# Kernel optimization log

Hardware: AMD Instinct MI355X
Metric: run time of the kernel (lower is better)

The kernel has to match this reference:

```python
import jax, jax.numpy as jnp
import numpy as np

NEG_INF = -jnp.inf


def setup_inputs() -> dict:
    B, T, D = 2, 512, 256
    key = jax.random.key(0)
    ks = jax.random.split(key, 12)
    inp = {
        'x': jax.random.normal(ks[0], (B, T, D), jnp.float32),
        'last_x': jnp.zeros((B, 1, D), jnp.float32),
        'last_num': jnp.zeros((B, 1, D), jnp.float32),
        'last_den': jnp.zeros((B, 1, D), jnp.float32),
        'time_decay': jax.random.normal(ks[1], (D,), jnp.float32) * 0.5,
        'time_first': jax.random.normal(ks[2], (D,), jnp.float32) * 0.5,
        'time_mix_k': jax.random.uniform(ks[3], (1, 1, D), jnp.float32),
        'time_mix_v': jax.random.uniform(ks[4], (1, 1, D), jnp.float32),
        'time_mix_r': jax.random.uniform(ks[5], (1, 1, D), jnp.float32),
        'Wk': jax.random.normal(ks[6], (D, D), jnp.float32) * 0.02,
        'Wv': jax.random.normal(ks[7], (D, D), jnp.float32) * 0.02,
        'Wr': jax.random.normal(ks[8], (D, D), jnp.float32) * 0.02,
        'Wo': jax.random.normal(ks[9], (D, D), jnp.float32) * 0.02,
    }
    return inp


def reference(x, last_x, last_num, last_den, time_decay, time_first,
              time_mix_k, time_mix_v, time_mix_r, Wk, Wv, Wr, Wo):
    B, T, D = x.shape

    # time_shift: prepend last_x, drop last step
    xs = jnp.concatenate([last_x, x[:, :-1, :]], axis=1)  # (B,T,D)

    k = (x * time_mix_k + xs * (1.0 - time_mix_k)) @ Wk.T
    v = (x * time_mix_v + xs * (1.0 - time_mix_v)) @ Wv.T
    r = (x * time_mix_r + xs * (1.0 - time_mix_r)) @ Wr.T
    sr = jax.nn.sigmoid(r)

    # --- run_wkv (quadratic exp-masked formulation, faithful to source) ---
    w = -jnp.exp(time_decay)                      # (D,)
    t = jnp.arange(T + 1, dtype=x.dtype)
    # wt[i, j] = j - i
    wt = t[None, :T] - t[:T, None]                # (T,T)
    tw = w[None, :] * t[1:, None]                 # (T,D): w * (j+1)
    twt = w[None, None, :] * wt[:, :, None]       # (T,T,D)
    # causal mask: -inf where j < i (strictly lower triangle, tril_(-1))
    ii = jnp.arange(T)
    mask = jnp.where(ii[:, None] > ii[None, :], NEG_INF, 0.0).astype(x.dtype)
    ktw = twt[None] + k[:, :, None, :] + mask[None, :, :, None]  # (B,T,T,D)
    etw = jnp.exp(tw)                             # (T,D)
    ektw = jnp.exp(ktw)                           # (B,T,T,D)
    num = etw[None] * last_num + jnp.einsum('bijd,bid->bjd', ektw, v)  # (B,T,D)
    den = etw[None] * last_den + ektw.sum(axis=1)                      # (B,T,D)
    num_prev = jnp.concatenate([last_num, num[:, :-1, :]], axis=1)
    den_prev = jnp.concatenate([last_den, den[:, :-1, :]], axis=1)
    euk = jnp.exp(time_first[None, None, :] + k)
    wkv = (num_prev + euk * v) / (den_prev + euk)
    # ----------------------------------------------------------------------

    out = (wkv * sr) @ Wo.T
    return (out, x[:, -1:, :], num[:, -1:, :], den[:, -1:, :])
```

## Files before the change

### kernel.cpp

```cpp
#include <hip/hip_runtime.h>

#define TT 512
#define DD 256
#define BB 2
#define MM (BB*TT)
#define LCH 8

__global__ __launch_bounds__(256)
void gemm_mix_t(const float* __restrict__ X, const float* __restrict__ Xlast,
                const float* __restrict__ W0, const float* __restrict__ W1,
                const float* __restrict__ W2,
                const float* __restrict__ mx0, const float* __restrict__ mx1,
                const float* __restrict__ mx2,
                float* __restrict__ O0, float* __restrict__ O1,
                float* __restrict__ O2)
{
    const int mat = blockIdx.z;
    const float* W  = (mat == 0) ? W0  : (mat == 1) ? W1  : W2;
    const float* mx = (mat == 0) ? mx0 : (mat == 1) ? mx1 : mx2;
    float*       O  = (mat == 0) ? O0  : (mat == 1) ? O1  : O2;

    const int n0   = blockIdx.x * 32;
    const int m0   = blockIdx.y * 32;
    const int b    = m0 / TT;
    const int t0   = m0 % TT;
    const int tid  = threadIdx.x;
    const int wv   = tid >> 6;
    const int lane = tid & 63;

    const int cc = (lane & 7) * 4;
    const int g  = lane >> 3;
    const int tm = lane >> 3;
    const int tn = lane & 7;

    __shared__ float As[4][32][36];
    __shared__ float Bs[4][32][36];

    const int kb = wv * 64;

    float4 a[4], w4[4];
    auto load_chunk = [&](int k0) {
        const float4 mv = *(const float4*)&mx[k0 + cc];
        #pragma unroll
        for (int i = 0; i < 4; ++i) {
            const int rr  = g + 8 * i;
            const int row = m0 + rr;
            const float4 xc = *(const float4*)&X[(size_t)row * DD + k0 + cc];
            float4 xp;
            if (t0 + rr == 0) xp = *(const float4*)&Xlast[b * DD + k0 + cc];
            else              xp = *(const float4*)&X[(size_t)(row - 1) * DD + k0 + cc];
            a[i].x = xp.x + (xc.x - xp.x) * mv.x;
            a[i].y = xp.y + (xc.y - xp.y) * mv.y;
            a[i].z = xp.z + (xc.z - xp.z) * mv.z;
            a[i].w = xp.w + (xc.w - xp.w) * mv.w;
            w4[i] = *(const float4*)&W[(size_t)(n0 + rr) * DD + k0 + cc];
        }
    };

    float acc[4][4] = {};
    load_chunk(kb);

    #pragma unroll
    for (int c = 0; c < 2; ++c) {
        #pragma unroll
        for (int i = 0; i < 4; ++i) {
            const int rr = g + 8 * i;
            As[wv][cc + 0][rr] = a[i].x; As[wv][cc + 1][rr] = a[i].y;
            As[wv][cc + 2][rr] = a[i].z; As[wv][cc + 3][rr] = a[i].w;
            Bs[wv][cc + 0][rr] = w4[i].x; Bs[wv][cc + 1][rr] = w4[i].y;
            Bs[wv][cc + 2][rr] = w4[i].z; Bs[wv][cc + 3][rr] = w4[i].w;
        }
        if (c == 0) load_chunk(kb + 32);
        #pragma unroll
        for (int kk = 0; kk < 32; ++kk) {
            const float4 a4 = *(const float4*)&As[wv][kk][tm * 4];
            const float4 b4 = *(const float4*)&Bs[wv][kk][tn * 4];
            const float am[4] = {a4.x, a4.y, a4.z, a4.w};
            const float bn[4] = {b4.x, b4.y, b4.z, b4.w};
            #pragma unroll
            for (int i = 0; i < 4; ++i)
                #pragma unroll
                for (int j = 0; j < 4; ++j)
                    acc[i][j] = fmaf(am[i], bn[j], acc[i][j]);
        }
    }

    if (wv != 0) {
        float* park = &As[wv][0][0];
        #pragma unroll
        for (int i = 0; i < 4; ++i)
            *(float4*)&park[(i * 64 + lane) * 4] =
                make_float4(acc[i][0], acc[i][1], acc[i][2], acc[i][3]);
    }
    __syncthreads();
    if (wv == 0) {
        #pragma unroll
        for (int w = 1; w < 4; ++w) {
            const float* park = &As[w][0][0];
            #pragma unroll
            for (int i = 0; i < 4; ++i) {
                const float4 o = *(const float4*)&park[(i * 64 + lane) * 4];
                acc[i][0] += o.x; acc[i][1] += o.y;
                acc[i][2] += o.z; acc[i][3] += o.w;
            }
        }
        #pragma unroll
        for (int j = 0; j < 4; ++j) {
            const float4 o = make_float4(acc[0][j], acc[1][j], acc[2][j], acc[3][j]);
            *(float4*)&O[(size_t)(b * DD + n0 + tn * 4 + j) * TT + t0 + tm * 4] = o;
        }
    }
}

__global__ __launch_bounds__(128)
void wkv_scan(const float* __restrict__ kT, const float* __restrict__ vT,
              const float* __restrict__ rT, const float* __restrict__ x,
              const float* __restrict__ last_num, const float* __restrict__ last_den,
              const float* __restrict__ time_decay, const float* __restrict__ time_first,
              float* __restrict__ yT, float* __restrict__ out)
{
    const int tid  = threadIdx.x;
    const int ch   = blockIdx.x * 2 + (tid >> 6);
    const int lane = tid & 63;
    const int b    = ch >> 8;
    const int d    = ch & (DD - 1);

    const float w  = -__expf(time_decay[d]);
    const float ew = __expf(w);
    const float eu = __expf(time_first[d]);

    const size_t base = (size_t)ch * TT + lane * LCH;
    float k_[LCH], v_[LCH], r_[LCH];
    #pragma unroll
    for (int i = 0; i < LCH / 4; ++i) {
        *(float4*)&k_[4 * i] = *(const float4*)(kT + base + 4 * i);
        *(float4*)&v_[4 * i] = *(const float4*)(vT + base + 4 * i);
        *(float4*)&r_[4 * i] = *(const float4*)(rT + base + 4 * i);
    }

    float ek[LCH], ekv[LCH], sr[LCH];
    #pragma unroll
    for (int i = 0; i < LCH; ++i) {
        ek[i]  = __expf(k_[i]);
        ekv[i] = ek[i] * v_[i];
        sr[i]  = __builtin_amdgcn_rcpf(1.0f + __expf(-r_[i]));
    }

    float A = __expf(w * (float)LCH);
    float Bn = 0.0f, Bd = 0.0f;
    #pragma unroll
    for (int i = 0; i < LCH; ++i) {
        Bn = fmaf(ew, Bn, ekv[i]);
        Bd = fmaf(ew, Bd, ek[i]);
    }

    #pragma unroll
    for (int s = 1; s < 64; s <<= 1) {
        const float Ax  = __shfl_up(A, s, 64);
        const float Bnx = __shfl_up(Bn, s, 64);
        const float Bdx = __shfl_up(Bd, s, 64);
        if (lane >= s) {
            Bn = fmaf(A, Bnx, Bn);
            Bd = fmaf(A, Bdx, Bd);
            A *= Ax;
        }
    }

    float Aex  = __shfl_up(A, 1, 64);
    float Bnex = __shfl_up(Bn, 1, 64);
    float Bdex = __shfl_up(Bd, 1, 64);
    if (lane == 0) { Aex = 1.0f; Bnex = 0.0f; Bdex = 0.0f; }
    float sn = fmaf(Aex, last_num[ch], Bnex);
    float sd = fmaf(Aex, last_den[ch], Bdex);

    float y_[LCH];
    #pragma unroll
    for (int i = 0; i < LCH; ++i) {
        const float euk = eu * ek[i];
        const float wkv = (sn + eu * ekv[i]) * __builtin_amdgcn_rcpf(sd + euk);
        y_[i] = wkv * sr[i];
        sn = fmaf(ew, sn, ekv[i]);
        sd = fmaf(ew, sd, ek[i]);
    }
    #pragma unroll
    for (int i = 0; i < LCH / 4; ++i)
        *(float4*)(yT + base + 4 * i) = *(const float4*)&y_[4 * i];

    if (lane == 63) {
        out[MM * DD + BB * DD + ch]     = sn;
        out[MM * DD + 2 * BB * DD + ch] = sd;
    }
    if (lane == 0)
        out[MM * DD + ch] = x[(b * TT + TT - 1) * DD + d];
}

__global__ __launch_bounds__(256)
void gemm_out(const float* __restrict__ yT, const float* __restrict__ Wo,
              float* __restrict__ O)
{
    const int n0   = blockIdx.x * 32;
    const int m0   = blockIdx.y * 32;
    const int b    = m0 >> 9;
    const int t0   = m0 & (TT - 1);
    const int tid  = threadIdx.x;
    const int wv   = tid >> 6;
    const int lane = tid & 63;

    __shared__ float As[4][2][32][40];
    __shared__ float Bs[4][2][32][36];

    const int tm = lane >> 3;
    const int tn = lane & 7;
    const int kr = lane >> 3;
    const int mq = (lane & 7) * 4;
    const int cc = (lane & 7) * 4;
    const int g  = lane >> 3;

    const int kb = wv * 64;

    float4 av[4], wv4[4];
    auto load_chunk = [&](int k0) {
        #pragma unroll
        for (int i = 0; i < 4; ++i)
            av[i] = *(const float4*)&yT[(size_t)(b * DD + k0 + kr + 8 * i) * TT + t0 + mq];
        #pragma unroll
        for (int i = 0; i < 4; ++i)
            wv4[i] = *(const float4*)&Wo[(size_t)(n0 + g + 8 * i) * DD + k0 + cc];
    };

    float acc[4][4] = {};
    load_chunk(kb);

    #pragma unroll
    for (int c = 0; c < 2; ++c) {
        const int buf = c & 1;
        #pragma unroll
        for (int i = 0; i < 4; ++i)
            *(float4*)&As[wv][buf][kr + 8 * i][mq] = av[i];
        #pragma unroll
        for (int i = 0; i < 4; ++i) {
            const int rr = g + 8 * i;
            Bs[wv][buf][cc + 0][rr] = wv4[i].x; Bs[wv][buf][cc + 1][rr] = wv4[i].y;
            Bs[wv][buf][cc + 2][rr] = wv4[i].z; Bs[wv][buf][cc + 3][rr] = wv4[i].w;
        }
        if (c == 0) load_chunk(kb + 32);
        #pragma unroll
        for (int kk = 0; kk < 32; ++kk) {
            const float4 a4 = *(const float4*)&As[wv][buf][kk][tm * 4];
            const float4 b4 = *(const float4*)&Bs[wv][buf][kk][tn * 4];
            const float am[4] = {a4.x, a4.y, a4.z, a4.w};
            const float bn[4] = {b4.x, b4.y, b4.z, b4.w};
            #pragma unroll
            for (int i = 0; i < 4; ++i)
                #pragma unroll
                for (int j = 0; j < 4; ++j)
                    acc[i][j] = fmaf(am[i], bn[j], acc[i][j]);
        }
    }

    if (wv != 0) {
        float* park = &As[wv][0][0][0];
        #pragma unroll
        for (int i = 0; i < 4; ++i)
            *(float4*)&park[lane * 20 + i * 4] =
                make_float4(acc[i][0], acc[i][1], acc[i][2], acc[i][3]);
    }
    __syncthreads();
    if (wv == 0) {
        #pragma unroll
        for (int w = 1; w < 4; ++w) {
            const float* park = &As[w][0][0][0];
            #pragma unroll
            for (int i = 0; i < 4; ++i) {
                const float4 o = *(const float4*)&park[lane * 20 + i * 4];
                acc[i][0] += o.x; acc[i][1] += o.y;
                acc[i][2] += o.z; acc[i][3] += o.w;
            }
        }
        #pragma unroll
        for (int i = 0; i < 4; ++i)
            *(float4*)&O[(size_t)(m0 + tm * 4 + i) * DD + n0 + tn * 4] =
                make_float4(acc[i][0], acc[i][1], acc[i][2], acc[i][3]);
    }
}

extern "C" void kernel_launch(void* const* d_in, const int* in_sizes, int n_in,
                              void* d_out, int out_size, void* d_ws, size_t ws_size,
                              hipStream_t stream)
{
    const float* x    = (const float*)d_in[0];
    const float* lx   = (const float*)d_in[1];
    const float* lnum = (const float*)d_in[2];
    const float* lden = (const float*)d_in[3];
    const float* td   = (const float*)d_in[4];
    const float* tf   = (const float*)d_in[5];
    const float* mk   = (const float*)d_in[6];
    const float* mv   = (const float*)d_in[7];
    const float* mr   = (const float*)d_in[8];
    const float* Wk   = (const float*)d_in[9];
    const float* Wv   = (const float*)d_in[10];
    const float* Wr   = (const float*)d_in[11];
    const float* Wo   = (const float*)d_in[12];
    float* out = (float*)d_out;

    float* kT = (float*)d_ws;
    float* vT = kT + MM * DD;
    float* rT = vT + MM * DD;
    float* yT = rT + MM * DD;

    gemm_mix_t<<<dim3(8, 32, 3), 256, 0, stream>>>(
        x, lx, Wk, Wv, Wr, mk, mv, mr, kT, vT, rT);

    wkv_scan<<<dim3(256), 128, 0, stream>>>(
        kT, vT, rT, x, lnum, lden, td, tf, yT, out);

    gemm_out<<<dim3(8, 32), 256, 0, stream>>>(yT, Wo, out);
}
```

Before: 99.11 us.

## Use packed FP32 FMA in GEMMs and split WKV scan across two wavefronts

Both GEMM inner loops now use inline-asm v_pk_fma_f32, which does two FMAs per instruction through op_sel broadcasting, with accumulators held as float2 pairs. This is meant to halve the VALU issue count in the FMA-bound inner loops. The WKV scan now gives each channel two wavefronts of 4 timesteps per lane instead of one wavefront of 8, and combines the two halves through a small shared-memory carry and a block barrier. This raises parallelism and shortens per-thread serial work, at the cost of an extra sync and more launched threads.

```diff
diff --git a/kernel.cpp b/kernel.cpp
--- a/kernel.cpp
+++ b/kernel.cpp
@@ -4,7 +4,13 @@
 #define DD 256
 #define BB 2
 #define MM (BB*TT)
-#define LCH 8
+
+#define PK_LO(acc, a, b) \
+    asm("v_pk_fma_f32 %0, %1, %2, %0 op_sel:[0,0,0] op_sel_hi:[0,1,1]" \
+        : "+v"(acc) : "v"(a), "v"(b))
+#define PK_HI(acc, a, b) \
+    asm("v_pk_fma_f32 %0, %1, %2, %0 op_sel:[1,0,0] op_sel_hi:[1,1,1]" \
+        : "+v"(acc) : "v"(a), "v"(b))
 
 __global__ __launch_bounds__(256)
 void gemm_mix_t(const float* __restrict__ X, const float* __restrict__ Xlast,
@@ -57,7 +63,7 @@
         }
     };
 
-    float acc[4][4] = {};
+    float2 acc2[4][2] = {};
     load_chunk(kb);
 
     #pragma unroll
@@ -73,15 +79,14 @@
         if (c == 0) load_chunk(kb + 32);
         #pragma unroll
         for (int kk = 0; kk < 32; ++kk) {
-            const float4 a4 = *(const float4*)&As[wv][kk][tm * 4];
-            const float4 b4 = *(const float4*)&Bs[wv][kk][tn * 4];
-            const float am[4] = {a4.x, a4.y, a4.z, a4.w};
-            const float bn[4] = {b4.x, b4.y, b4.z, b4.w};
-            #pragma unroll
-            for (int i = 0; i < 4; ++i)
-                #pragma unroll
-                for (int j = 0; j < 4; ++j)
-                    acc[i][j] = fmaf(am[i], bn[j], acc[i][j]);
+            const float2 a01 = *(const float2*)&As[wv][kk][tm * 4];
+            const float2 a23 = *(const float2*)&As[wv][kk][tm * 4 + 2];
+            const float2 b01 = *(const float2*)&Bs[wv][kk][tn * 4];
+            const float2 b23 = *(const float2*)&Bs[wv][kk][tn * 4 + 2];
+            PK_LO(acc2[0][0], a01, b01); PK_LO(acc2[0][1], a01, b23);
+            PK_HI(acc2[1][0], a01, b01); PK_HI(acc2[1][1], a01, b23);
+            PK_LO(acc2[2][0], a23, b01); PK_LO(acc2[2][1], a23, b23);
+            PK_HI(acc2[3][0], a23, b01); PK_HI(acc2[3][1], a23, b23);
         }
     }
 
@@ -90,7 +95,7 @@
         #pragma unroll
         for (int i = 0; i < 4; ++i)
             *(float4*)&park[(i * 64 + lane) * 4] =
-                make_float4(acc[i][0], acc[i][1], acc[i][2], acc[i][3]);
+                make_float4(acc2[i][0].x, acc2[i][0].y, acc2[i][1].x, acc2[i][1].y);
     }
     __syncthreads();
     if (wv == 0) {
@@ -100,19 +105,22 @@
             #pragma unroll
             for (int i = 0; i < 4; ++i) {
                 const float4 o = *(const float4*)&park[(i * 64 + lane) * 4];
-                acc[i][0] += o.x; acc[i][1] += o.y;
-                acc[i][2] += o.z; acc[i][3] += o.w;
+                acc2[i][0].x += o.x; acc2[i][0].y += o.y;
+                acc2[i][1].x += o.z; acc2[i][1].y += o.w;
             }
         }
-        #pragma unroll
-        for (int j = 0; j < 4; ++j) {
-            const float4 o = make_float4(acc[0][j], acc[1][j], acc[2][j], acc[3][j]);
-            *(float4*)&O[(size_t)(b * DD + n0 + tn * 4 + j) * TT + t0 + tm * 4] = o;
-        }
+        const float4 oj0 = make_float4(acc2[0][0].x, acc2[1][0].x, acc2[2][0].x, acc2[3][0].x);
+        const float4 oj1 = make_float4(acc2[0][0].y, acc2[1][0].y, acc2[2][0].y, acc2[3][0].y);
+        const float4 oj2 = make_float4(acc2[0][1].x, acc2[1][1].x, acc2[2][1].x, acc2[3][1].x);
+        const float4 oj3 = make_float4(acc2[0][1].y, acc2[1][1].y, acc2[2][1].y, acc2[3][1].y);
+        *(float4*)&O[(size_t)(b * DD + n0 + tn * 4 + 0) * TT + t0 + tm * 4] = oj0;
+        *(float4*)&O[(size_t)(b * DD + n0 + tn * 4 + 1) * TT + t0 + tm * 4] = oj1;
+        *(float4*)&O[(size_t)(b * DD + n0 + tn * 4 + 2) * TT + t0 + tm * 4] = oj2;
+        *(float4*)&O[(size_t)(b * DD + n0 + tn * 4 + 3) * TT + t0 + tm * 4] = oj3;
     }
 }
 
-__global__ __launch_bounds__(128)
+__global__ __launch_bounds__(256)
 void wkv_scan(const float* __restrict__ kT, const float* __restrict__ vT,
               const float* __restrict__ rT, const float* __restrict__ x,
               const float* __restrict__ last_num, const float* __restrict__ last_den,
@@ -120,8 +128,10 @@
               float* __restrict__ yT, float* __restrict__ out)
 {
     const int tid  = threadIdx.x;
-    const int ch   = blockIdx.x * 2 + (tid >> 6);
+    const int chl  = tid >> 7;
+    const int half = (tid >> 6) & 1;
     const int lane = tid & 63;
+    const int ch   = blockIdx.x * 2 + chl;
     const int b    = ch >> 8;
     const int d    = ch & (DD - 1);
 
@@ -129,27 +139,26 @@
     const float ew = __expf(w);
     const float eu = __expf(time_first[d]);
 
-    const size_t base = (size_t)ch * TT + lane * LCH;
-    float k_[LCH], v_[LCH], r_[LCH];
-    #pragma unroll
-    for (int i = 0; i < LCH / 4; ++i) {
-        *(float4*)&k_[4 * i] = *(const float4*)(kT + base + 4 * i);
-        *(float4*)&v_[4 * i] = *(const float4*)(vT + base + 4 * i);
-        *(float4*)&r_[4 * i] = *(const float4*)(rT + base + 4 * i);
-    }
-
-    float ek[LCH], ekv[LCH], sr[LCH];
-    #pragma unroll
-    for (int i = 0; i < LCH; ++i) {
+    const size_t base = (size_t)ch * TT + half * (TT / 2) + lane * 4;
+    const float4 k4 = *(const float4*)(kT + base);
+    const float4 v4 = *(const float4*)(vT + base);
+    const float4 r4 = *(const float4*)(rT + base);
+    const float k_[4] = {k4.x, k4.y, k4.z, k4.w};
+    const float v_[4] = {v4.x, v4.y, v4.z, v4.w};
+    const float r_[4] = {r4.x, r4.y, r4.z, r4.w};
+
+    float ek[4], ekv[4], sr[4];
+    #pragma unroll
+    for (int i = 0; i < 4; ++i) {
         ek[i]  = __expf(k_[i]);
         ekv[i] = ek[i] * v_[i];
         sr[i]  = __builtin_amdgcn_rcpf(1.0f + __expf(-r_[i]));
     }
 
-    float A = __expf(w * (float)LCH);
+    float A = __expf(w * 4.0f);
     float Bn = 0.0f, Bd = 0.0f;
     #pragma unroll
-    for (int i = 0; i < LCH; ++i) {
+    for (int i = 0; i < 4; ++i) {
         Bn = fmaf(ew, Bn, ekv[i]);
         Bd = fmaf(ew, Bd, ek[i]);
     }
@@ -166,31 +175,40 @@
         }
     }
 
+    __shared__ float h[2][3];
+    if (half == 0 && lane == 63) { h[chl][0] = A; h[chl][1] = Bn; h[chl][2] = Bd; }
+
     float Aex  = __shfl_up(A, 1, 64);
     float Bnex = __shfl_up(Bn, 1, 64);
     float Bdex = __shfl_up(Bd, 1, 64);
     if (lane == 0) { Aex = 1.0f; Bnex = 0.0f; Bdex = 0.0f; }
-    float sn = fmaf(Aex, last_num[ch], Bnex);
-    float sd = fmaf(Aex, last_den[ch], Bdex);
-
-    float y_[LCH];
-    #pragma unroll
-    for (int i = 0; i < LCH; ++i) {
+
+    __syncthreads();
+
+    float s0n = last_num[ch], s0d = last_den[ch];
+    if (half == 1) {
+        s0n = fmaf(h[chl][0], s0n, h[chl][1]);
+        s0d = fmaf(h[chl][0], s0d, h[chl][2]);
+    }
+    float sn = fmaf(Aex, s0n, Bnex);
+    float sd = fmaf(Aex, s0d, Bdex);
+
+    float y_[4];
+    #pragma unroll
+    for (int i = 0; i < 4; ++i) {
         const float euk = eu * ek[i];
         const float wkv = (sn + eu * ekv[i]) * __builtin_amdgcn_rcpf(sd + euk);
         y_[i] = wkv * sr[i];
         sn = fmaf(ew, sn, ekv[i]);
         sd = fmaf(ew, sd, ek[i]);
     }
-    #pragma unroll
-    for (int i = 0; i < LCH / 4; ++i)
-        *(float4*)(yT + base + 4 * i) = *(const float4*)&y_[4 * i];
-
-    if (lane == 63) {
+    *(float4*)(yT + base) = make_float4(y_[0], y_[1], y_[2], y_[3]);
+
+    if (half == 1 && lane == 63) {
         out[MM * DD + BB * DD + ch]     = sn;
         out[MM * DD + 2 * BB * DD + ch] = sd;
     }
-    if (lane == 0)
+    if (half == 0 && lane == 0)
         out[MM * DD + ch] = x[(b * TT + TT - 1) * DD + d];
 }
 
@@ -228,7 +246,7 @@
             wv4[i] = *(const float4*)&Wo[(size_t)(n0 + g + 8 * i) * DD + k0 + cc];
     };
 
-    float acc[4][4] = {};
+    float2 acc2[4][2] = {};
     load_chunk(kb);
 
     #pragma unroll
@@ -246,15 +264,14 @@
         if (c == 0) load_chunk(kb + 32);
         #pragma unroll
         for (int kk = 0; kk < 32; ++kk) {
-            const float4 a4 = *(const float4*)&As[wv][buf][kk][tm * 4];
-            const float4 b4 = *(const float4*)&Bs[wv][buf][kk][tn * 4];
-            const float am[4] = {a4.x, a4.y, a4.z, a4.w};
-            const float bn[4] = {b4.x, b4.y, b4.z, b4.w};
-            #pragma unroll
-            for (int i = 0; i < 4; ++i)
-                #pragma unroll
-                for (int j = 0; j < 4; ++j)
-                    acc[i][j] = fmaf(am[i], bn[j], acc[i][j]);
+            const float2 a01 = *(const float2*)&As[wv][buf][kk][tm * 4];
+            const float2 a23 = *(const float2*)&As[wv][buf][kk][tm * 4 + 2];
+            const float2 b01 = *(const float2*)&Bs[wv][buf][kk][tn * 4];
+            const float2 b23 = *(const float2*)&Bs[wv][buf][kk][tn * 4 + 2];
+            PK_LO(acc2[0][0], a01, b01); PK_LO(acc2[0][1], a01, b23);
+            PK_HI(acc2[1][0], a01, b01); PK_HI(acc2[1][1], a01, b23);
+            PK_LO(acc2[2][0], a23, b01); PK_LO(acc2[2][1], a23, b23);
+            PK_HI(acc2[3][0], a23, b01); PK_HI(acc2[3][1], a23, b23);
         }
     }
 
@@ -263,7 +280,7 @@
         #pragma unroll
         for (int i = 0; i < 4; ++i)
             *(float4*)&park[lane * 20 + i * 4] =
-                make_float4(acc[i][0], acc[i][1], acc[i][2], acc[i][3]);
+                make_float4(acc2[i][0].x, acc2[i][0].y, acc2[i][1].x, acc2[i][1].y);
     }
     __syncthreads();
     if (wv == 0) {
@@ -273,14 +290,14 @@
             #pragma unroll
             for (int i = 0; i < 4; ++i) {
                 const float4 o = *(const float4*)&park[lane * 20 + i * 4];
-                acc[i][0] += o.x; acc[i][1] += o.y;
-                acc[i][2] += o.z; acc[i][3] += o.w;
+                acc2[i][0].x += o.x; acc2[i][0].y += o.y;
+                acc2[i][1].x += o.z; acc2[i][1].y += o.w;
             }
         }
         #pragma unroll
         for (int i = 0; i < 4; ++i)
             *(float4*)&O[(size_t)(m0 + tm * 4 + i) * DD + n0 + tn * 4] =
-                make_float4(acc[i][0], acc[i][1], acc[i][2], acc[i][3]);
+                make_float4(acc2[i][0].x, acc2[i][0].y, acc2[i][1].x, acc2[i][1].y);
     }
 }
 
@@ -311,7 +328,7 @@
     gemm_mix_t<<<dim3(8, 32, 3), 256, 0, stream>>>(
         x, lx, Wk, Wv, Wr, mk, mv, mr, kT, vT, rT);
 
-    wkv_scan<<<dim3(256), 128, 0, stream>>>(
+    wkv_scan<<<dim3(256), 256, 0, stream>>>(
         kT, vT, rT, x, lnum, lden, td, tf, yT, out);
 
     gemm_out<<<dim3(8, 32), 256, 0, stream>>>(yT, Wo, out);
```

Measured after the change: 97.03 us, median of 2. -2.1%, faster.
